# Kernel tuning notes

Measured on AMD Instinct MI355X. Metric: run time of the kernel, lower is better.

The kernel has to match this reference:

```python
import jax, jax.numpy as jnp
import numpy as np

NUM_AGENT = 200
LOOK_BACK = 10
NUM_CTRL = 9
DIM = 512
HEADS = 8
DIM_HEAD = 64
N = NUM_AGENT * LOOK_BACK + NUM_CTRL  # 2009
BATCH = 4
SCALE = DIM_HEAD ** -0.5


def _build_mask():
    # eye(num_agent) repeat_interleaved by look_back on rows and cols == kron with ones(lb,lb)
    m = jnp.kron(jnp.eye(NUM_AGENT, dtype=jnp.float32),
                 jnp.ones((LOOK_BACK, LOOK_BACK), jnp.float32))
    # pad with zeros for the control-feature rows/cols
    return jnp.pad(m, ((0, NUM_CTRL), (0, NUM_CTRL)))  # [N, N]


def _split_heads(t):
    b, n, hd = t.shape
    return t.reshape(b, n, HEADS, hd // HEADS).transpose(0, 2, 1, 3)  # [b,h,n,d]


def setup_inputs() -> dict:
    key = jax.random.key(0)
    ks = jax.random.split(key, 5)
    inner = HEADS * DIM_HEAD
    return {
        "x": jax.random.normal(ks[0], (BATCH, N, DIM), jnp.float32),
        "w_qkv": jax.random.normal(ks[1], (DIM, inner * 3), jnp.float32) * 0.02,
        "w_qk_self": jax.random.normal(ks[2], (DIM, inner * 2), jnp.float32) * 0.02,
        "w_out": jax.random.normal(ks[3], (inner, DIM), jnp.float32) * 0.02,
        "b_out": jnp.zeros((DIM,), jnp.float32),
    }


def reference(x, w_qkv, w_qk_self, w_out, b_out):
    mask = _build_mask()  # [N, N], broadcasts over [b, h]
    q, k, v = map(_split_heads, jnp.split(x @ w_qkv, 3, axis=-1))
    q_s, k_s = map(_split_heads, jnp.split(x @ w_qk_self, 2, axis=-1))
    dots = jnp.einsum('bhnd,bhmd->bhnm', q, k) * SCALE
    dots_self = jnp.einsum('bhnd,bhmd->bhnm', q_s, k_s) * SCALE
    blended = mask * dots_self + (1.0 - mask) * dots
    attn = jax.nn.softmax(blended, axis=-1)  # [b,h,n,n]
    out = jnp.einsum('bhnm,bhmd->bhnd', attn, v)
    out = out.transpose(0, 2, 1, 3).reshape(x.shape[0], N, HEADS * DIM_HEAD)
    return out @ w_out + b_out, attn
```

## Files before the change

### kernel.cpp

```cpp
#include <hip/hip_runtime.h>
#include <hip/hip_bf16.h>


#define N_TOK   2009
#define NPAD    2048
#define NTILES  16
#define NT2     32
#define BATCH_  4
#define HEADS_  8
#define MROWS   8036
#define SCALE_  0.125f
#define RPB_A   256
#define RPV     128
#define PFP     68

typedef __attribute__((ext_vector_type(8)))  short sh8;
typedef __attribute__((ext_vector_type(16))) float f32x16;

static inline int cdiv(int a, int b) { return (a + b - 1) / b; }

__device__ __forceinline__ float4 ld4(const float* p) {
    return *reinterpret_cast<const float4*>(p);
}
__device__ __forceinline__ unsigned short f2bf(float f) {
    __hip_bfloat16 h = __float2bfloat16(f);
    return *reinterpret_cast<unsigned short*>(&h);
}
__device__ __forceinline__ float bf2f(unsigned short u) {
    return __uint_as_float(((unsigned)u) << 16);
}
__device__ __forceinline__ void cvt8(const float4& a, const float4& b, sh8& hi, sh8& lo) {
    float f[8] = {a.x, a.y, a.z, a.w, b.x, b.y, b.z, b.w};
#pragma unroll
    for (int i = 0; i < 8; ++i) {
        unsigned short h = f2bf(f[i]);
        hi[i] = (short)h;
        lo[i] = (short)f2bf(f[i] - bf2f(h));
    }
}
__device__ __forceinline__ void cvt8p(const float4& a, const float4& b, sh8& hi) {
#pragma unroll
    for (int i = 0; i < 4; ++i) {
        hi[i]     = (short)f2bf((&a.x)[i]);
        hi[4 + i] = (short)f2bf((&b.x)[i]);
    }
}
typedef const __attribute__((address_space(1))) void gas_void;
typedef __attribute__((address_space(3))) void las_void;
__device__ __forceinline__ void gll16(const void* g, void* l) {
    __builtin_amdgcn_global_load_lds((gas_void*)g, (las_void*)l, 16, 0, 0);
}

__device__ __forceinline__ void bar_lds() {
    asm volatile("s_waitcnt lgkmcnt(0)" ::: "memory");
    __builtin_amdgcn_sched_barrier(0);
    __builtin_amdgcn_s_barrier();
    __builtin_amdgcn_sched_barrier(0);
}
__device__ __forceinline__ void bar_keep4() {
    asm volatile("s_waitcnt vmcnt(4) lgkmcnt(0)" ::: "memory");
    __builtin_amdgcn_sched_barrier(0);
    __builtin_amdgcn_s_barrier();
    __builtin_amdgcn_sched_barrier(0);
}

__global__ __launch_bounds__(256)
void convert_x(const float* __restrict__ x, unsigned short* __restrict__ xh,
               unsigned short* __restrict__ xl)
{
    const int mt = blockIdx.x;
    const int w  = threadIdx.x >> 6;
    const int kc = threadIdx.x & 63;
    for (int it = 0; it < 8; ++it) {
        int rg = it * 4 + w;
        sh8 hi[4], lo[4];
#pragma unroll
        for (int rr = 0; rr < 4; ++rr) {
            int row = rg * 4 + rr;
            int gm = mt * 128 + row;
            int b = gm >> 11, gr = gm & 2047;
            float4 a = make_float4(0.f, 0.f, 0.f, 0.f), c = a;
            if (gr < N_TOK) {
                const float* p = x + ((size_t)b * N_TOK + gr) * 512 + kc * 8;
                a = ld4(p); c = ld4(p + 4);
            }
            cvt8(a, c, hi[rr], lo[rr]);
        }
        size_t base = ((size_t)(mt * 64 + kc) * 128 + rg * 4) * 8;
#pragma unroll
        for (int rr = 0; rr < 4; ++rr) {
            *reinterpret_cast<sh8*>(xh + base + rr * 8) = hi[rr];
            *reinterpret_cast<sh8*>(xl + base + rr * 8) = lo[rr];
        }
    }
}

__global__ __launch_bounds__(256)
void convert_w(const float* __restrict__ wqkv, const float* __restrict__ wself,
               const float* __restrict__ wout,
               unsigned short* __restrict__ qh, unsigned short* __restrict__ ql,
               unsigned short* __restrict__ sh, unsigned short* __restrict__ sl,
               unsigned short* __restrict__ oh, unsigned short* __restrict__ ol)
{
    int cid = blockIdx.x * 256 + threadIdx.x;
    int nt_all = cid >> 13, rem = cid & 8191;
    int kc = rem >> 7, col = rem & 127;
    const float* src; unsigned short *dh, *dl; int Nn, ntl;
    if (nt_all < 12)      { src = wqkv;  dh = qh; dl = ql; Nn = 1536; ntl = nt_all; }
    else if (nt_all < 20) { src = wself; dh = sh; dl = sl; Nn = 1024; ntl = nt_all - 12; }
    else                  { src = wout;  dh = oh; dl = ol; Nn = 512;  ntl = nt_all - 20; }
    float f[8];
#pragma unroll
    for (int i = 0; i < 8; ++i)
        f[i] = src[(size_t)(kc * 8 + i) * Nn + ntl * 128 + col];
    sh8 hi, lo;
    cvt8(make_float4(f[0], f[1], f[2], f[3]), make_float4(f[4], f[5], f[6], f[7]), hi, lo);
    size_t off = ((size_t)(ntl * 64 + kc) * 128 + col) * 8;
    *reinterpret_cast<sh8*>(dh + off) = hi;
    *reinterpret_cast<sh8*>(dl + off) = lo;
}

template<int MODE>
__global__ __launch_bounds__(512)
void gemm_bf16(const unsigned short* __restrict__ Ah, const unsigned short* __restrict__ Al,
               const unsigned short* __restrict__ Bh, const unsigned short* __restrict__ Bl,
               float* __restrict__ C, const float* __restrict__ bias)
{
    __shared__ __align__(16) unsigned short AhS[2][4096], AlS[2][4096],
                                            BhS[2][4096], BlS[2][4096];
    const int tid = threadIdx.x, lane = tid & 63, wid = tid >> 6;
    const int mt = blockIdx.x, ntile = blockIdx.y;
    const int wm = wid >> 2, wn = wid & 3;
    const int lj = lane & 31, g = lane >> 5;

    const unsigned short* Asrc_h = Ah + (size_t)mt * 65536;
    const unsigned short* Asrc_l = Al + (size_t)mt * 65536;
    const unsigned short* Bsrc_h = Bh + (size_t)ntile * 65536;
    const unsigned short* Bsrc_l = Bl + (size_t)ntile * 65536;

#define GSTAGE(BUF, S) do {                                                      \
    gll16(Asrc_h + (size_t)(S) * 4096 + tid * 8, (char*)AhS[BUF] + tid * 16);    \
    gll16(Asrc_l + (size_t)(S) * 4096 + tid * 8, (char*)AlS[BUF] + tid * 16);    \
    gll16(Bsrc_h + (size_t)(S) * 4096 + tid * 8, (char*)BhS[BUF] + tid * 16);    \
    gll16(Bsrc_l + (size_t)(S) * 4096 + tid * 8, (char*)BlS[BUF] + tid * 16);    \
} while (0)

    f32x16 acc[2];
#pragma unroll
    for (int i = 0; i < 16; ++i) { acc[0][i] = 0.f; acc[1][i] = 0.f; }

    GSTAGE(0, 0);
    for (int s = 0; s < 16; ++s) {
        const int buf = s & 1;
        __syncthreads();
        if (s + 1 < 16) GSTAGE(buf ^ 1, s + 1);
#pragma unroll
        for (int ks = 0; ks < 2; ++ks) {
            const int kcl = 2 * ks + g;
            sh8 bh = *reinterpret_cast<const sh8*>(BhS[buf] + (kcl * 128 + wn * 32 + lj) * 8);
            sh8 bl = *reinterpret_cast<const sh8*>(BlS[buf] + (kcl * 128 + wn * 32 + lj) * 8);
#pragma unroll
            for (int Mt = 0; Mt < 2; ++Mt) {
                sh8 ah = *reinterpret_cast<const sh8*>(AhS[buf] + (kcl * 128 + wm * 64 + Mt * 32 + lj) * 8);
                sh8 al = *reinterpret_cast<const sh8*>(AlS[buf] + (kcl * 128 + wm * 64 + Mt * 32 + lj) * 8);
                acc[Mt] = __builtin_amdgcn_mfma_f32_32x32x16_bf16(ah, bh, acc[Mt], 0, 0, 0);
                acc[Mt] = __builtin_amdgcn_mfma_f32_32x32x16_bf16(ah, bl, acc[Mt], 0, 0, 0);
                acc[Mt] = __builtin_amdgcn_mfma_f32_32x32x16_bf16(al, bh, acc[Mt], 0, 0, 0);
            }
        }
    }
#undef GSTAGE

#pragma unroll
    for (int Mt = 0; Mt < 2; ++Mt) {
#pragma unroll
        for (int reg = 0; reg < 16; ++reg) {
            int rloc = wm * 64 + Mt * 32 + (reg & 3) + 8 * (reg >> 2) + 4 * g;
            int gm = mt * 128 + rloc;
            int b = gm >> 11, gr = gm & 2047;
            if (gr < N_TOK) {
                int coln = ntile * 128 + wn * 32 + lj;
                float v = acc[Mt][reg];
                size_t idx;
                if (MODE == 1)
                    idx = ((size_t)(coln >> 9) * MROWS + (size_t)b * N_TOK + gr) * 512 + (coln & 511);
                else if (MODE == 0)
                    idx = ((size_t)b * N_TOK + gr) * 1024 + coln;
                else {
                    v += bias[coln];
                    idx = ((size_t)b * N_TOK + gr) * 512 + coln;
                }
                C[idx] = v;
            }
        }
    }
}

__global__ __launch_bounds__(256)
void selfE_k(const float* __restrict__ proj2, float* __restrict__ selfE)
{
    __shared__ float qs[10][64];
    __shared__ float ks[10][68];
    const int a = blockIdx.x;
    const int h = blockIdx.y & 7;
    const int b = blockIdx.y >> 3;
    const size_t rowbase = (size_t)b * N_TOK + a * 10;

    for (int i = threadIdx.x; i < 320; i += 256) {
        int r = i >> 4;
        int c = (i & 15) * 4;
        const float* src = proj2 + (rowbase + (r % 10)) * 1024
                         + (r < 10 ? 0 : 512) + h * 64 + c;
        float4 v = ld4(src);
        if (r < 10) *reinterpret_cast<float4*>(&qs[r][c]) = v;
        else        *reinterpret_cast<float4*>(&ks[r - 10][c]) = v;
    }
    __syncthreads();
    if (threadIdx.x < 100) {
        int r = threadIdx.x / 10, c = threadIdx.x % 10;
        float acc = 0.f;
#pragma unroll 8
        for (int d = 0; d < 64; ++d) acc += qs[r][d] * ks[c][d];
        int bh = b * HEADS_ + h;
        selfE[((size_t)bh * 2000 + a * 10 + r) * 10 + c] = __expf(acc * SCALE_);
    }
}

__global__ __launch_bounds__(256)
void convert_kv(const float* __restrict__ Kf, const float* __restrict__ Vf,
                unsigned short* __restrict__ Khg, unsigned short* __restrict__ Klg,
                unsigned short* __restrict__ Vtg)
{
    __shared__ float vtile[128][66];
    const int t  = blockIdx.x;
    const int h  = blockIdx.y & 7;
    const int b  = blockIdx.y >> 3;
    const int bh = blockIdx.y;
    const size_t bN = (size_t)b * N_TOK;
    const size_t tbase = ((size_t)bh * NTILES + t) * 8192;
    const int tid = threadIdx.x;

    {
        int r = tid >> 1, q = tid & 1;
        int gj = t * 128 + r;
        float4 f[8];
        if (gj < N_TOK) {
            const float* kp = Kf + (bN + gj) * 512 + h * 64 + q * 32;
#pragma unroll
            for (int i = 0; i < 8; ++i) f[i] = ld4(kp + 4 * i);
        } else {
#pragma unroll
            for (int i = 0; i < 8; ++i) f[i] = make_float4(0.f, 0.f, 0.f, 0.f);
        }
#pragma unroll
        for (int cp = 0; cp < 4; ++cp) {
            sh8 hi, lo;
            cvt8(f[2 * cp], f[2 * cp + 1], hi, lo);
            int kc = q * 4 + cp;
            size_t off = tbase + ((size_t)kc * 128 + r) * 8;
            *reinterpret_cast<sh8*>(Khg + off) = hi;
            *reinterpret_cast<sh8*>(Klg + off) = lo;
        }
    }
    {
        int r = tid >> 1, q = tid & 1;
        int gj = t * 128 + r;
        const float* vp = Vf + (bN + gj) * 512 + h * 64 + q * 32;
#pragma unroll
        for (int i = 0; i < 8; ++i) {
            float4 v = (gj < N_TOK) ? ld4(vp + 4 * i) : make_float4(0.f, 0.f, 0.f, 0.f);
            *reinterpret_cast<float4*>(&vtile[r][q * 32 + 4 * i]) = v;
        }
    }
    __syncthreads();
    {
        int d = tid & 63, jg = tid >> 6;
#pragma unroll
        for (int jj = 0; jj < 4; ++jj) {
            int jc = jg * 4 + jj;
            sh8 pk;
#pragma unroll
            for (int i = 0; i < 8; ++i) pk[i] = (short)f2bf(vtile[jc * 8 + i][d]);
            *reinterpret_cast<sh8*>(Vtg + tbase + ((size_t)jc * 64 + d) * 8) = pk;
        }
    }
}

__global__ __launch_bounds__(512, 2)
void attn_rowsum(const float* __restrict__ Qf,
                 const unsigned short* __restrict__ Khg,
                 const float* __restrict__ selfE,
                 float* __restrict__ rowinv)
{
    __shared__ __align__(16) unsigned short KhS[2][8192];
    __shared__ float selfS[RPB_A * 10];

    const int bid = blockIdx.x;
    const int xcd = bid & 7, idx = bid >> 3;
    const int bh  = xcd * 4 + (idx >> 3);
    const int bx  = idx & 7;
    const int h = bh & 7, b = bh >> 3;
    const int tid = threadIdx.x, lane = tid & 63, wid = tid >> 6;
    const int row0 = bx * RPB_A;
    const int wr = wid * 32;
    const size_t bN = (size_t)b * N_TOK;
    const int lj = lane & 31, g = lane >> 5;

    for (int i = tid; i < RPB_A * 10; i += 512) {
        int r = i / 10, c = i - r * 10;
        int gr = row0 + r;
        selfS[i] = (gr < 2000) ? selfE[((size_t)bh * 2000 + gr) * 10 + c] : 0.f;
    }

    sh8 qh[4];
    {
        int grow = row0 + wr + lj;
        bool val = grow < N_TOK;
        const float* qp = Qf + (bN + (val ? grow : 0)) * 512 + h * 64;
#pragma unroll
        for (int ks = 0; ks < 4; ++ks) {
            int kc = 2 * ks + g;
            float4 a = val ? ld4(qp + kc * 8)     : make_float4(0.f, 0.f, 0.f, 0.f);
            float4 c = val ? ld4(qp + kc * 8 + 4) : make_float4(0.f, 0.f, 0.f, 0.f);
            cvt8p(a, c, qh[ks]);
        }
    }

    const unsigned short* ktiles = Khg + (size_t)bh * NTILES * 8192;
#define RSTAGE(T) do {                                                          \
    const unsigned short* kt = ktiles + (size_t)(T) * 8192;                     \
    char* dst = (char*)KhS[(T) & 1];                                            \
    _Pragma("unroll") for (int i = 0; i < 2; ++i)                               \
        gll16(kt + i * 4096 + tid * 8, dst + i * 8192 + tid * 16); } while (0)

    RSTAGE(0);

    float rsacc[16];
#pragma unroll
    for (int i = 0; i < 16; ++i) rsacc[i] = 0.f;

    const int alo = (row0 / 10) * 10;
    const int rmax = row0 + RPB_A - 1 < 1999 ? row0 + RPB_A - 1 : 1999;
    const int ahi = (rmax / 10) * 10 + 10;

    for (int t = 0; t < NTILES; ++t) {
        __syncthreads();
        if (t + 1 < NTILES) RSTAGE(t + 1);
        const unsigned short* kb = KhS[t & 1];
        const bool dtile = (alo < t * 128 + 128) && (ahi > t * 128);
#pragma unroll
        for (int ct = 0; ct < 4; ++ct) {
            sh8 kf[4];
#pragma unroll
            for (int ks = 0; ks < 4; ++ks)
                kf[ks] = *reinterpret_cast<const sh8*>(kb + ((2 * ks + g) * 128 + 32 * ct + lj) * 8);
            f32x16 s;
#pragma unroll
            for (int i = 0; i < 16; ++i) s[i] = 0.f;
#pragma unroll
            for (int ks = 0; ks < 4; ++ks)
                s = __builtin_amdgcn_mfma_f32_32x32x16_bf16(qh[ks], kf[ks], s, 0, 0, 0);
            const int gj = t * 128 + 32 * ct + lj;
            if (gj < N_TOK) {
#pragma unroll
                for (int reg = 0; reg < 16; ++reg) {
                    int rloc = wr + (reg & 3) + 8 * (reg >> 2) + 4 * g;
                    int grow = row0 + rloc;
                    float e = __expf(s[reg] * SCALE_);
                    if (dtile && grow < 2000) {
                        int a0 = (grow / 10) * 10;
                        unsigned cc = (unsigned)(gj - a0);
                        if (cc < 10u) e = selfS[rloc * 10 + (int)cc];
                    }
                    rsacc[reg] += e;
                }
            }
        }
    }
#undef RSTAGE

#pragma unroll
    for (int reg = 0; reg < 16; ++reg) {
        float v = rsacc[reg];
        v += __shfl_xor(v, 1);  v += __shfl_xor(v, 2);
        v += __shfl_xor(v, 4);  v += __shfl_xor(v, 8);
        v += __shfl_xor(v, 16);
        rsacc[reg] = v;
    }
    if (lj == 0) {
#pragma unroll
        for (int reg = 0; reg < 16; ++reg) {
            int rloc = wr + (reg & 3) + 8 * (reg >> 2) + 4 * g;
            int grow = row0 + rloc;
            rowinv[(size_t)bh * NPAD + row0 + rloc] =
                (grow < N_TOK) ? 1.0f / rsacc[reg] : 0.f;
        }
    }
}

__global__ __launch_bounds__(512, 2)
void attn_pv(const float* __restrict__ Qf,
             const unsigned short* __restrict__ Khg,
             const unsigned short* __restrict__ Klg,
             const unsigned short* __restrict__ Vtg,
             const float* __restrict__ selfE,
             const float* __restrict__ rowinv,
             float* __restrict__ attn,
             unsigned short* __restrict__ Ohg, unsigned short* __restrict__ Olg,
             float* __restrict__ dump)
{
    extern __shared__ __align__(16) char smem[];
    unsigned short* KhS = (unsigned short*)smem;
    unsigned short* KlS = KhS + 4096;
    unsigned short* VtS = KlS + 4096;
    float* Pf = (float*)(VtS + 8192);
    unsigned short* selfS = (unsigned short*)(Pf + RPV * PFP);
    float* rinvS = (float*)(selfS + RPV * 10);

    const int bid = blockIdx.x;
    const int xcd = bid & 7, idx = bid >> 3;
    const int bh  = xcd * 4 + (idx >> 4);
    const int bx  = idx & 15;
    const int h = bh & 7, b = bh >> 3;
    const int tid = threadIdx.x, lane = tid & 63, wid = tid >> 6;
    const int row0 = bx * RPV;
    const int wr = (wid & 3) * 32;
    const int cw = wid >> 2;
    const size_t bN = (size_t)b * N_TOK;
    const size_t abase = ((size_t)bh * N_TOK + row0) * N_TOK;
    const int lj = lane & 31, g = lane >> 5;
    float* dumpT = dump + ((size_t)bh * 512 + tid) * 4;

    for (int i = tid; i < RPV * 10; i += 512) {
        int r = i / 10, c = i - r * 10;
        int gr = row0 + r;
        selfS[i] = (gr < 2000) ? f2bf(selfE[((size_t)bh * 2000 + gr) * 10 + c]) : 0;
    }
    if (tid < RPV) rinvS[tid] = rowinv[(size_t)bh * NPAD + row0 + tid];

    sh8 qh[4], ql[4];
    {
        int grow = row0 + wr + lj;
        bool val = grow < N_TOK;
        const float* qp = Qf + (bN + (val ? grow : 0)) * 512 + h * 64;
#pragma unroll
        for (int ks = 0; ks < 4; ++ks) {
            int kc = 2 * ks + g;
            float4 a = val ? ld4(qp + kc * 8)     : make_float4(0.f, 0.f, 0.f, 0.f);
            float4 c = val ? ld4(qp + kc * 8 + 4) : make_float4(0.f, 0.f, 0.f, 0.f);
            cvt8(a, c, qh[ks], ql[ks]);
        }
    }

    const unsigned short* khT = Khg + (size_t)bh * NTILES * 8192;
    const unsigned short* klT = Klg + (size_t)bh * NTILES * 8192;
    const unsigned short* vtT = Vtg + (size_t)bh * NTILES * 8192;

#define STAGE_KH(T) gll16(khT + (size_t)((T) >> 1) * 8192                           \
        + ((size_t)(tid >> 6) * 128 + 64 * ((T) & 1) + (tid & 63)) * 8,             \
        (char*)KhS + tid * 16)
#define STAGE_KL(T) gll16(klT + (size_t)((T) >> 1) * 8192                           \
        + ((size_t)(tid >> 6) * 128 + 64 * ((T) & 1) + (tid & 63)) * 8,             \
        (char*)KlS + tid * 16)
#define STAGE_VT(T) gll16(vtT + (size_t)((T) >> 1) * 8192                           \
        + ((size_t)(8 * ((T) & 1) + (tid >> 6)) * 64 + (tid & 63)) * 8,             \
        (char*)(VtS + ((T) & 1) * 4096) + tid * 16)

#define QK_PHASE(T) do {                                                            \
        const bool dtile = (alo < (T) * 64 + 64) && (ahi > (T) * 64);               \
        sh8 kfh[4], kfl[4];                                                         \
        _Pragma("unroll") for (int ks = 0; ks < 4; ++ks) {                          \
            int off = ((2 * ks + g) * 64 + 32 * cw + lj) * 8;                       \
            kfh[ks] = *reinterpret_cast<const sh8*>(KhS + off);                     \
            kfl[ks] = *reinterpret_cast<const sh8*>(KlS + off);                     \
        }                                                                           \
        f32x16 s;                                                                   \
        _Pragma("unroll") for (int i = 0; i < 16; ++i) s[i] = 0.f;                  \
        _Pragma("unroll") for (int ks = 0; ks < 4; ++ks) {                          \
            s = __builtin_amdgcn_mfma_f32_32x32x16_bf16(qh[ks], kfh[ks], s, 0,0,0); \
            s = __builtin_amdgcn_mfma_f32_32x32x16_bf16(qh[ks], kfl[ks], s, 0,0,0); \
            s = __builtin_amdgcn_mfma_f32_32x32x16_bf16(ql[ks], kfh[ks], s, 0,0,0); \
        }                                                                           \
        const int cin = 32 * cw + lj;                                               \
        const int gj  = (T) * 64 + cin;                                             \
        const bool jv = gj < N_TOK;                                                 \
        _Pragma("unroll") for (int reg = 0; reg < 16; ++reg) {                      \
            int rowl = (reg & 3) + 8 * (reg >> 2) + 4 * g;                          \
            int rloc = wr + rowl;                                                   \
            int grow = row0 + rloc;                                                 \
            float e = 0.f;                                                          \
            if (jv && grow < N_TOK) e = __expf(s[reg] * SCALE_);                    \
            if (dtile && jv && grow < 2000) {                                       \
                int a0 = (grow / 10) * 10;                                          \
                unsigned cc = (unsigned)(gj - a0);                                  \
                if (cc < 10u) e = bf2f(selfS[rloc * 10 + (int)cc]);                 \
            }                                                                       \
            Pf[rloc * PFP + cin] = e * rinvS[rloc];                                 \
        }                                                                           \
    } while (0)

#define PV_PHASE(T) do {                                                            \
        const unsigned short* vtb = VtS + ((T) & 1) * 4096;                         \
        _Pragma("unroll") for (int m = 0; m < 4; ++m) {                             \
            const float* pp = &Pf[(wr + lj) * PFP + 16 * m + 8 * g];                \
            float4 a = ld4(pp), b4 = ld4(pp + 4);                                   \
            sh8 pa; cvt8p(a, b4, pa);                                               \
            sh8 vf = *reinterpret_cast<const sh8*>(                                 \
                vtb + ((2 * m + g) * 64 + 32 * cw + lj) * 8);                       \
            oacc = __builtin_amdgcn_mfma_f32_32x32x16_bf16(pa, vf, oacc, 0, 0, 0);  \
        }                                                                           \
    } while (0)

    STAGE_KH(0); STAGE_KL(0); STAGE_VT(0);

    const int alo = (row0 / 10) * 10;
    const int rmax = row0 + RPV - 1 < 1999 ? row0 + RPV - 1 : 1999;
    const int ahi = (rmax / 10) * 10 + 10;

    f32x16 oacc;
#pragma unroll
    for (int i = 0; i < 16; ++i) oacc[i] = 0.f;

    __syncthreads();

    for (int t = 0; t < NT2 - 1; ++t) {
        QK_PHASE(t);
        bar_lds();
        STAGE_KH(t + 1); STAGE_KL(t + 1); STAGE_VT(t + 1);
        {
            const int c4  = (tid & 15) * 4;
            const int gj0 = t * 64 + c4;
#pragma unroll
            for (int it = 0; it < 4; ++it) {
                int r = it * 32 + (tid >> 4);
                int grow = row0 + r;
                float4 v = ld4(&Pf[r * PFP + c4]);
                float* ap = attn + abase + (size_t)r * N_TOK + gj0;
                float* sdst = (grow < N_TOK) ? ap : dumpT;
                *reinterpret_cast<float4*>(sdst) = v;
            }
        }
        PV_PHASE(t);
        bar_keep4();
    }

    {
        const int t = NT2 - 1;
        QK_PHASE(t);
        __syncthreads();
        PV_PHASE(t);
        {
            const int c4  = (tid & 15) * 4;
            const int gj0 = t * 64 + c4;
#pragma unroll
            for (int it = 0; it < 4; ++it) {
                int r = it * 32 + (tid >> 4);
                int grow = row0 + r;
                if (grow < N_TOK) {
                    float4 v = ld4(&Pf[r * PFP + c4]);
                    float* ap = attn + abase + (size_t)r * N_TOK + gj0;
                    if (gj0 + 3 < N_TOK) {
                        *reinterpret_cast<float4*>(ap) = v;
                    } else {
#pragma unroll
                        for (int e = 0; e < 4; ++e)
                            if (gj0 + e < N_TOK) ap[e] = (&v.x)[e];
                    }
                }
            }
        }
        __syncthreads();
    }
#undef STAGE_KH
#undef STAGE_KL
#undef STAGE_VT
#undef QK_PHASE
#undef PV_PHASE

    float* Ofull = (float*)smem;
#pragma unroll
    for (int reg = 0; reg < 16; ++reg) {
        int rloc = wr + (reg & 3) + 8 * (reg >> 2) + 4 * g;
        Ofull[rloc * 68 + 32 * cw + lj] = oacc[reg];
    }
    __syncthreads();
#pragma unroll
    for (int it = 0; it < 2; ++it) {
        int task = it * 512 + tid;
        int row = task >> 3, kq = task & 7;
        const float* op = Ofull + row * 68 + kq * 8;
        float4 a = ld4(op), c = ld4(op + 4);
        sh8 hi, lo; cvt8(a, c, hi, lo);
        int gm = b * 2048 + row0 + row;
        int mtile = gm >> 7, row128 = gm & 127;
        size_t off = ((size_t)(mtile * 64 + h * 8 + kq) * 128 + row128) * 8;
        *reinterpret_cast<sh8*>(Ohg + off) = hi;
        *reinterpret_cast<sh8*>(Olg + off) = lo;
    }
}

extern "C" void kernel_launch(void* const* d_in, const int* in_sizes, int n_in,
                              void* d_out, int out_size, void* d_ws, size_t ws_size,
                              hipStream_t stream)
{
    const float* x         = (const float*)d_in[0];
    const float* w_qkv     = (const float*)d_in[1];
    const float* w_qk_self = (const float*)d_in[2];
    const float* w_out     = (const float*)d_in[3];
    const float* b_out     = (const float*)d_in[4];

    float* out  = (float*)d_out;
    float* attn = out + (size_t)MROWS * 512;

    float* Qf = (float*)d_ws;
    float* Kf = Qf + (size_t)MROWS * 512;
    float* Vf = Kf + (size_t)MROWS * 512;
    float* p2 = Vf + (size_t)MROWS * 512;
    unsigned short* Khg = (unsigned short*)p2;
    unsigned short* Klg = Khg + 4194304;
    unsigned short* Vtg = Klg + 4194304;
    float* proj2 = p2;
    float* after_p2 = p2 + (size_t)MROWS * 1024;
    unsigned short* xh  = (unsigned short*)after_p2;
    unsigned short* xl  = xh + 4194304;
    unsigned short* Wqh = xl + 4194304;
    unsigned short* Wql = Wqh + 786432;
    unsigned short* Wsh = Wql + 786432;
    unsigned short* Wsl = Wsh + 524288;
    unsigned short* Woh = Wsl + 524288;
    unsigned short* Wol = Woh + 262144;
    float* rowinv = (float*)(Wol + 262144);
    float* selfE  = rowinv + 65536;
    float* dump   = selfE + 640000;
    unsigned short* Ohg = (unsigned short*)Kf;
    unsigned short* Olg = Ohg + 4194304;

    const int smem_pv = 8192 + 8192 + 16384
                      + RPV * PFP * 4
                      + RPV * 10 * 2 + RPV * 4;
    hipFuncSetAttribute((const void*)attn_pv,
                        hipFuncAttributeMaxDynamicSharedMemorySize, smem_pv);

    convert_x<<<64, 256, 0, stream>>>(x, xh, xl);
    convert_w<<<768, 256, 0, stream>>>(w_qkv, w_qk_self, w_out,
                                       Wqh, Wql, Wsh, Wsl, Woh, Wol);

    dim3 g1(64, 12);
    gemm_bf16<1><<<g1, 512, 0, stream>>>(xh, xl, Wqh, Wql, Qf, nullptr);

    dim3 g2(64, 8);
    gemm_bf16<0><<<g2, 512, 0, stream>>>(xh, xl, Wsh, Wsl, proj2, nullptr);

    dim3 gs(200, 32);
    selfE_k<<<gs, 256, 0, stream>>>(proj2, selfE);

    dim3 gc(NTILES, 32);
    convert_kv<<<gc, 256, 0, stream>>>(Kf, Vf, Khg, Klg, Vtg);

    attn_rowsum<<<256, 512, 0, stream>>>(Qf, Khg, selfE, rowinv);

    attn_pv<<<512, 512, smem_pv, stream>>>(Qf, Khg, Klg, Vtg, selfE, rowinv,
                                           attn, Ohg, Olg, dump);

    dim3 g3(64, 4);
    gemm_bf16<2><<<g3, 512, 0, stream>>>(Ohg, Olg, Woh, Wol, out, b_out);
}
```

Before: 474.2 us.

## Store attention probabilities as per-wave coalesced scalar rows and split convert_x grid

The attention-probability writeback changes from unaligned float4 stores, which are misaligned because the row stride is 2009, to per-wave scalar stores where each wave writes 16 full 64-column rows. Each store instruction is therefore a contiguous 256-byte segment. The barrier's vmcnt wait is raised to 16 to match the larger number of outstanding stores, and the dump pointer is redirected. Separately, convert_x launches 4x more blocks so more CUs are used. The trade-off is more store instructions per thread against fewer partial or misaligned transactions.

Measured after the change: 469.5 us. About the same (-1.0%).

```diff
diff --git a/kernel.cpp b/kernel.cpp
--- a/kernel.cpp
+++ b/kernel.cpp
@@ -57,8 +57,8 @@
     __builtin_amdgcn_s_barrier();
     __builtin_amdgcn_sched_barrier(0);
 }
-__device__ __forceinline__ void bar_keep4() {
-    asm volatile("s_waitcnt vmcnt(4) lgkmcnt(0)" ::: "memory");
+__device__ __forceinline__ void bar_keep16() {
+    asm volatile("s_waitcnt vmcnt(16) lgkmcnt(0)" ::: "memory");
     __builtin_amdgcn_sched_barrier(0);
     __builtin_amdgcn_s_barrier();
     __builtin_amdgcn_sched_barrier(0);
@@ -69,10 +69,11 @@
                unsigned short* __restrict__ xl)
 {
     const int mt = blockIdx.x;
+    const int yq = blockIdx.y;
     const int w  = threadIdx.x >> 6;
     const int kc = threadIdx.x & 63;
-    for (int it = 0; it < 8; ++it) {
-        int rg = it * 4 + w;
+    for (int it = 0; it < 2; ++it) {
+        int rg = (yq * 2 + it) * 4 + w;
         sh8 hi[4], lo[4];
 #pragma unroll
         for (int rr = 0; rr < 4; ++rr) {
@@ -429,7 +430,7 @@
     const size_t bN = (size_t)b * N_TOK;
     const size_t abase = ((size_t)bh * N_TOK + row0) * N_TOK;
     const int lj = lane & 31, g = lane >> 5;
-    float* dumpT = dump + ((size_t)bh * 512 + tid) * 4;
+    float* dumpT = dump + ((size_t)(bid & 511) << 6) + lane;
 
     for (int i = tid; i < RPV * 10; i += 512) {
         int r = i / 10, c = i - r * 10;
@@ -523,25 +524,25 @@
 
     __syncthreads();
 
+    const int rbase = wid * 16;
+
     for (int t = 0; t < NT2 - 1; ++t) {
         QK_PHASE(t);
         bar_lds();
         STAGE_KH(t + 1); STAGE_KL(t + 1); STAGE_VT(t + 1);
         {
-            const int c4  = (tid & 15) * 4;
-            const int gj0 = t * 64 + c4;
-#pragma unroll
-            for (int it = 0; it < 4; ++it) {
-                int r = it * 32 + (tid >> 4);
+            float* ap0 = attn + abase + (size_t)t * 64 + lane;
+#pragma unroll
+            for (int i = 0; i < 16; ++i) {
+                int r = rbase + i;
                 int grow = row0 + r;
-                float4 v = ld4(&Pf[r * PFP + c4]);
-                float* ap = attn + abase + (size_t)r * N_TOK + gj0;
-                float* sdst = (grow < N_TOK) ? ap : dumpT;
-                *reinterpret_cast<float4*>(sdst) = v;
+                float v = Pf[r * PFP + lane];
+                float* sdst = (grow < N_TOK) ? (ap0 + (size_t)r * N_TOK) : dumpT;
+                *sdst = v;
             }
         }
         PV_PHASE(t);
-        bar_keep4();
+        bar_keep16();
     }
 
     {
@@ -549,24 +550,14 @@
         QK_PHASE(t);
         __syncthreads();
         PV_PHASE(t);
-        {
-            const int c4  = (tid & 15) * 4;
-            const int gj0 = t * 64 + c4;
-#pragma unroll
-            for (int it = 0; it < 4; ++it) {
-                int r = it * 32 + (tid >> 4);
+        if (t * 64 + lane < N_TOK) {
+            float* ap0 = attn + abase + (size_t)t * 64 + lane;
+#pragma unroll
+            for (int i = 0; i < 16; ++i) {
+                int r = rbase + i;
                 int grow = row0 + r;
-                if (grow < N_TOK) {
-                    float4 v = ld4(&Pf[r * PFP + c4]);
-                    float* ap = attn + abase + (size_t)r * N_TOK + gj0;
-                    if (gj0 + 3 < N_TOK) {
-                        *reinterpret_cast<float4*>(ap) = v;
-                    } else {
-#pragma unroll
-                        for (int e = 0; e < 4; ++e)
-                            if (gj0 + e < N_TOK) ap[e] = (&v.x)[e];
-                    }
-                }
+                if (grow < N_TOK)
+                    ap0[(size_t)r * N_TOK] = Pf[r * PFP + lane];
             }
         }
         __syncthreads();
@@ -641,7 +632,8 @@
     hipFuncSetAttribute((const void*)attn_pv,
                         hipFuncAttributeMaxDynamicSharedMemorySize, smem_pv);
 
-    convert_x<<<64, 256, 0, stream>>>(x, xh, xl);
+    dim3 gx(64, 4);
+    convert_x<<<gx, 256, 0, stream>>>(x, xh, xl);
     convert_w<<<768, 256, 0, stream>>>(w_qkv, w_qk_self, w_out,
                                        Wqh, Wql, Wsh, Wsl, Woh, Wol);
 
```
